# Optimization experiments

Measured on AMD Instinct MI355X. Metric: run time of the kernel, lower is better.

The kernel has to match this reference:

```python
import jax, jax.numpy as jnp
import numpy as np

DIM = 1024
H = 16
D = DIM // H  # head_dim = 64
SCALE = 1.0 / (D ** 0.5 * 1.0)  # 1/(sqrt(head_dim)*temperature)
MIN_CUTOFF = 1e-15


def setup_inputs() -> dict:
    key = jax.random.key(0)
    ks = jax.random.split(key, 6)
    B, T = 2, 2048
    x = jax.random.normal(ks[0], (B, T, DIM), dtype=jnp.float32)
    cutoffs = jax.random.uniform(ks[1], (B, T, T), dtype=jnp.float32)
    # torch nn.Linear params: weight [out, in], bias [out]
    W_qkv = jax.random.normal(ks[2], (3 * DIM, DIM), dtype=jnp.float32) * (DIM ** -0.5)
    b_qkv = jax.random.normal(ks[3], (3 * DIM,), dtype=jnp.float32) * 0.01
    W_out = jax.random.normal(ks[4], (DIM, DIM), dtype=jnp.float32) * (DIM ** -0.5)
    b_out = jax.random.normal(ks[5], (DIM,), dtype=jnp.float32) * 0.01
    return {"x": x, "cutoffs": cutoffs, "W_qkv": W_qkv, "b_qkv": b_qkv,
            "W_out": W_out, "b_out": b_out}


def reference(x, cutoffs, W_qkv, b_qkv, W_out, b_out):
    B, T, _ = x.shape
    # QKV projection -> [B, T, 3, H, D] -> [3, B, H, T, D]
    qkv = (jnp.einsum('btc,oc->bto', x, W_qkv) + b_qkv)
    qkv = qkv.reshape(B, T, 3, H, D).transpose(2, 0, 3, 1, 4)
    q, k, v = qkv[0], qkv[1], qkv[2]
    # additive log-bias from cutoffs, broadcast over heads
    bias = jnp.log(jnp.clip(cutoffs, MIN_CUTOFF, None))[:, None, :, :]  # [B,1,T,T]
    scores = jnp.einsum('bhqd,bhkd->bhqk', q, k) * SCALE + bias
    attn = jax.nn.softmax(scores, axis=-1)
    out = jnp.einsum('bhqk,bhkd->bhqd', attn, v)  # [B,H,T,D]
    out = out.transpose(0, 2, 1, 3).reshape(B, T, DIM)
    return jnp.einsum('btc,oc->bto', out, W_out) + b_out
```

## Files before the change

### kernel.cpp

```cpp
#include <hip/hip_runtime.h>

typedef __attribute__((ext_vector_type(4))) float f32x4;
typedef __attribute__((ext_vector_type(8))) short bf16x8;

__device__ __forceinline__ unsigned short f2bf(float f) {
    union { float f; unsigned u; } v; v.f = f;
    unsigned r = v.u + 0x7FFFu + ((v.u >> 16) & 1u);
    return (unsigned short)(r >> 16);
}
__device__ __forceinline__ float bf2f(unsigned short s) {
    union { unsigned u; float f; } v; v.u = ((unsigned)s) << 16;
    return v.f;
}

#define GLD16(gp, lp)                                                          \
    __builtin_amdgcn_global_load_lds(                                          \
        (const __attribute__((address_space(1))) void*)(gp),                   \
        (__attribute__((address_space(3))) void*)(lp), 16, 0, 0)

__global__ void k_cvt(const float* __restrict__ in, unsigned short* __restrict__ out, int n4) {
    int i = blockIdx.x * blockDim.x + threadIdx.x;
    int stride = gridDim.x * blockDim.x;
    for (; i < n4; i += stride) {
        float4 v = reinterpret_cast<const float4*>(in)[i];
        ushort4 o;
        o.x = f2bf(v.x); o.y = f2bf(v.y); o.z = f2bf(v.z); o.w = f2bf(v.w);
        reinterpret_cast<ushort4*>(out)[i] = o;
    }
}

__global__ void k_cvtc(const float* __restrict__ in, unsigned short* __restrict__ out, int n4) {
    int i = blockIdx.x * blockDim.x + threadIdx.x;
    int stride = gridDim.x * blockDim.x;
    for (; i < n4; i += stride) {
        float4 v = reinterpret_cast<const float4*>(in)[i];
        ushort4 o;
        o.x = f2bf(fmaxf(v.x, 1e-15f)); o.y = f2bf(fmaxf(v.y, 1e-15f));
        o.z = f2bf(fmaxf(v.z, 1e-15f)); o.w = f2bf(fmaxf(v.w, 1e-15f));
        reinterpret_cast<ushort4*>(out)[i] = o;
    }
}

template <int MODE>
__global__ __launch_bounds__(256) void gemm_bt(
    const unsigned short* __restrict__ A, const unsigned short* __restrict__ B,
    const float* __restrict__ bias, float* __restrict__ outf,
    unsigned short* __restrict__ qb, unsigned short* __restrict__ kb,
    unsigned short* __restrict__ vb, int M, int N, int K)
{
    __shared__ unsigned short sA[2][128 * 32];
    __shared__ unsigned short sB[2][128 * 32];
    const int tid = threadIdx.x;
    const int w = tid >> 6, lane = tid & 63, g = lane >> 4, r = lane & 15;
    const int tm = blockIdx.x * 128, tn = blockIdx.y * 128;
    const int wr = w >> 1, wc = w & 1;

    f32x4 acc[4][4];
#pragma unroll
    for (int i = 0; i < 4; i++)
#pragma unroll
        for (int j = 0; j < 4; j++) acc[i][j] = (f32x4)0.f;

    const unsigned short* ga0 = A + (size_t)(tm + w * 32 + (lane >> 2)) * K + (lane & 3) * 8;
    const unsigned short* gb0 = B + (size_t)(tn + w * 32 + (lane >> 2)) * K + (lane & 3) * 8;
    const int lbase = w * 32 * 32;

    auto stageAB = [&](int nb, int kk) {
        GLD16(ga0 + kk, &sA[nb][lbase]);
        GLD16(ga0 + kk + (size_t)16 * K, &sA[nb][lbase + 16 * 32]);
        GLD16(gb0 + kk, &sB[nb][lbase]);
        GLD16(gb0 + kk + (size_t)16 * K, &sB[nb][lbase + 16 * 32]);
    };

    stageAB(0, 0);
    __syncthreads();

#pragma unroll 2
    for (int kk = 0; kk < K; kk += 32) {
        const int cur = (kk >> 5) & 1;
        if (kk + 32 < K) stageAB(cur ^ 1, kk + 32);
        bf16x8 af[4], bfv[4];
#pragma unroll
        for (int f = 0; f < 4; f++) af[f] = *(const bf16x8*)&sA[cur][(wr * 64 + f * 16 + r) * 32 + g * 8];
#pragma unroll
        for (int f = 0; f < 4; f++) bfv[f] = *(const bf16x8*)&sB[cur][(wc * 64 + f * 16 + r) * 32 + g * 8];
#pragma unroll
        for (int i = 0; i < 4; i++)
#pragma unroll
            for (int j = 0; j < 4; j++)
                acc[i][j] = __builtin_amdgcn_mfma_f32_16x16x32_bf16(af[i], bfv[j], acc[i][j], 0, 0, 0);
        __syncthreads();
    }

#pragma unroll
    for (int fj = 0; fj < 4; fj++) {
        int n = tn + wc * 64 + fj * 16 + r;
        float bn = bias[n];
#pragma unroll
        for (int fi = 0; fi < 4; fi++) {
#pragma unroll
            for (int j = 0; j < 4; j++) {
                int m = tm + wr * 64 + fi * 16 + 4 * g + j;
                float v = acc[fi][fj][j] + bn;
                if (MODE == 0) {
                    outf[(size_t)m * N + n] = v;
                } else {
                    int three = n >> 10, h = (n >> 6) & 15, d = n & 63;
                    int b = m >> 11, t = m & 2047, bh = b * 16 + h;
                    if (three == 0) {
                        qb[((size_t)bh * 2048 + t) * 64 + d] = f2bf(v * 0.18033688f);
                    } else if (three == 1) {
                        kb[((size_t)bh * 2048 + t) * 64 + d] = f2bf(v);
                    } else {
                        vb[((size_t)bh * 64 + d) * 2048 + t] = f2bf(v);
                    }
                }
            }
        }
    }
}

__global__ __launch_bounds__(256) void attn_kernel(
    const unsigned short* __restrict__ qbuf, const unsigned short* __restrict__ kbuf,
    const unsigned short* __restrict__ vbuf, const unsigned short* __restrict__ cutb,
    unsigned short* __restrict__ outa)
{
    __shared__ unsigned short sK[64 * 64], sV[64 * 64], sP[4 * 16 * 64];
    const int tid = threadIdx.x, w = tid >> 6, lane = tid & 63, g = lane >> 4, r = lane & 15;
    const int qt = blockIdx.x, h = blockIdx.y, b = blockIdx.z;
    const int q0 = qt * 64, bh = b * 16 + h;

    bf16x8 aq[2];
    {
        const unsigned short* qp = qbuf + ((size_t)bh * 2048 + q0 + w * 16 + r) * 64;
        aq[0] = *(const bf16x8*)(qp + g * 8);
        aq[1] = *(const bf16x8*)(qp + 32 + g * 8);
    }

    const int c = lane & 7, rr = lane >> 3;
    auto stage = [&](int kt) {
#pragma unroll
        for (int i = 0; i < 2; i++) {
            int row = w * 16 + i * 8 + rr;
            GLD16(kbuf + ((size_t)bh * 2048 + kt * 64 + row) * 64 + (c ^ (row & 7)) * 8,
                  sK + (w * 16 + i * 8) * 64);
            GLD16(vbuf + ((size_t)bh * 64 + row) * 2048 + kt * 64 + (c ^ (row & 7)) * 8,
                  sV + (w * 16 + i * 8) * 64);
        }
    };

    const unsigned short* cp[4];
#pragma unroll
    for (int j = 0; j < 4; j++)
        cp[j] = cutb + ((size_t)b * 2048 + (q0 + w * 16 + 4 * g + j)) * 2048 + r;

    f32x4 oacc[4];
#pragma unroll
    for (int f = 0; f < 4; f++) oacc[f] = (f32x4)0.f;
    float psum[4] = {0.f, 0.f, 0.f, 0.f};

    unsigned short* sPw = sP + w * 16 * 64;

    for (int kt = 0; kt < 32; kt++) {
        __syncthreads();
        stage(kt);
        unsigned short cu[4][4];
#pragma unroll
        for (int f = 0; f < 4; f++)
#pragma unroll
            for (int j = 0; j < 4; j++) cu[f][j] = cp[j][kt * 64 + f * 16];
        __syncthreads();

        f32x4 sa[4];
#pragma unroll
        for (int f = 0; f < 4; f++) sa[f] = (f32x4)0.f;
#pragma unroll
        for (int s = 0; s < 2; s++)
#pragma unroll
            for (int f = 0; f < 4; f++) {
                int krow = f * 16 + r;
                bf16x8 bk = *(const bf16x8*)&sK[krow * 64 + ((s * 32 + g * 8) ^ ((krow & 7) << 3))];
                sa[f] = __builtin_amdgcn_mfma_f32_16x16x32_bf16(aq[s], bk, sa[f], 0, 0, 0);
            }

#pragma unroll
        for (int f = 0; f < 4; f++)
#pragma unroll
            for (int j = 0; j < 4; j++) {
                float p = bf2f(cu[f][j]) * exp2f(sa[f][j]);
                psum[j] += p;
                int row = 4 * g + j, col = f * 16 + r;
                sPw[row * 64 + (col ^ ((row & 7) << 3))] = f2bf(p);
            }

#pragma unroll
        for (int s = 0; s < 2; s++) {
            bf16x8 pa = *(const bf16x8*)&sPw[r * 64 + ((s * 32 + g * 8) ^ ((r & 7) << 3))];
#pragma unroll
            for (int f = 0; f < 4; f++) {
                int drow = f * 16 + r;
                bf16x8 bvv = *(const bf16x8*)&sV[drow * 64 + ((s * 32 + g * 8) ^ ((drow & 7) << 3))];
                oacc[f] = __builtin_amdgcn_mfma_f32_16x16x32_bf16(pa, bvv, oacc[f], 0, 0, 0);
            }
        }
    }

#pragma unroll
    for (int j = 0; j < 4; j++) {
        psum[j] += __shfl_xor(psum[j], 1);
        psum[j] += __shfl_xor(psum[j], 2);
        psum[j] += __shfl_xor(psum[j], 4);
        psum[j] += __shfl_xor(psum[j], 8);
    }

#pragma unroll
    for (int j = 0; j < 4; j++) {
        float inv = 1.f / psum[j];
        int q = q0 + w * 16 + 4 * g + j;
#pragma unroll
        for (int f = 0; f < 4; f++) {
            int d = f * 16 + r;
            outa[((size_t)(b * 2048 + q)) * 1024 + h * 64 + d] = f2bf(oacc[f][j] * inv);
        }
    }
}

extern "C" void kernel_launch(void* const* d_in, const int* in_sizes, int n_in,
                              void* d_out, int out_size, void* d_ws, size_t ws_size,
                              hipStream_t stream) {
    const float* x       = (const float*)d_in[0];
    const float* cutoffs = (const float*)d_in[1];
    const float* Wqkv    = (const float*)d_in[2];
    const float* bqkv    = (const float*)d_in[3];
    const float* Wout    = (const float*)d_in[4];
    const float* bout    = (const float*)d_in[5];
    float* out = (float*)d_out;

    char* ws = (char*)d_ws;
    unsigned short* x_bf    = (unsigned short*)ws;  ws += (size_t)4096 * 1024 * 2;
    unsigned short* wqkv_bf = (unsigned short*)ws;  ws += (size_t)3072 * 1024 * 2;
    unsigned short* wout_bf = (unsigned short*)ws;  ws += (size_t)1024 * 1024 * 2;
    unsigned short* qb      = (unsigned short*)ws;  ws += (size_t)32 * 2048 * 64 * 2;
    unsigned short* kb      = (unsigned short*)ws;  ws += (size_t)32 * 2048 * 64 * 2;
    unsigned short* vb      = (unsigned short*)ws;  ws += (size_t)32 * 2048 * 64 * 2;
    unsigned short* attn_o  = (unsigned short*)ws;  ws += (size_t)4096 * 1024 * 2;
    unsigned short* cutb    = (unsigned short*)ws;  ws += (size_t)2 * 2048 * 2048 * 2;

    k_cvt<<<1024, 256, 0, stream>>>(x,    x_bf,    4096 * 1024 / 4);
    k_cvt<<<1024, 256, 0, stream>>>(Wqkv, wqkv_bf, 3072 * 1024 / 4);
    k_cvt<<<512,  256, 0, stream>>>(Wout, wout_bf, 1024 * 1024 / 4);
    k_cvtc<<<2048, 256, 0, stream>>>(cutoffs, cutb, 2 * 2048 * 2048 / 4);

    gemm_bt<1><<<dim3(32, 24), 256, 0, stream>>>(x_bf, wqkv_bf, bqkv, nullptr,
                                                 qb, kb, vb, 4096, 3072, 1024);
    attn_kernel<<<dim3(32, 16, 2), 256, 0, stream>>>(qb, kb, vb, cutb, attn_o);
    gemm_bt<0><<<dim3(32, 8), 256, 0, stream>>>(attn_o, wout_bf, bout, out,
                                                nullptr, nullptr, nullptr, 4096, 1024, 1024);
}
```

Before: 255.5 us.

## Double-buffer K/V tiles in attention, add MFMA priority, shrink out-proj GEMM tile

The attention kernel now double-buffers its K and V shared-memory tiles, prefetching the next tile while computing on the current one. This removes one barrier per iteration and overlaps global loads with MFMA work. The GEMM keeps a single barrier per k-step and raises wave priority with s_setprio around the MFMA blocks. The output projection uses a 64-row M tile, giving 512 blocks instead of 256 for better CU coverage. In exchange, attention uses more LDS, which may lower occupancy, and the barrier moves to the top of the GEMM loop.

```diff
diff --git a/kernel.cpp b/kernel.cpp
--- a/kernel.cpp
+++ b/kernel.cpp
@@ -41,55 +41,59 @@
     }
 }
 
-template <int MODE>
+template <int MODE, int BM>
 __global__ __launch_bounds__(256) void gemm_bt(
     const unsigned short* __restrict__ A, const unsigned short* __restrict__ B,
     const float* __restrict__ bias, float* __restrict__ outf,
     unsigned short* __restrict__ qb, unsigned short* __restrict__ kb,
     unsigned short* __restrict__ vb, int M, int N, int K)
 {
-    __shared__ unsigned short sA[2][128 * 32];
+    constexpr int FM = BM / 32;
+    __shared__ unsigned short sA[2][BM * 32];
     __shared__ unsigned short sB[2][128 * 32];
     const int tid = threadIdx.x;
     const int w = tid >> 6, lane = tid & 63, g = lane >> 4, r = lane & 15;
-    const int tm = blockIdx.x * 128, tn = blockIdx.y * 128;
+    const int tm = blockIdx.x * BM, tn = blockIdx.y * 128;
     const int wr = w >> 1, wc = w & 1;
 
-    f32x4 acc[4][4];
-#pragma unroll
-    for (int i = 0; i < 4; i++)
+    f32x4 acc[FM][4];
+#pragma unroll
+    for (int i = 0; i < FM; i++)
 #pragma unroll
         for (int j = 0; j < 4; j++) acc[i][j] = (f32x4)0.f;
 
-    const unsigned short* ga0 = A + (size_t)(tm + w * 32 + (lane >> 2)) * K + (lane & 3) * 8;
+    const unsigned short* ga0 = A + (size_t)(tm + w * (BM / 4) + (lane >> 2)) * K + (lane & 3) * 8;
     const unsigned short* gb0 = B + (size_t)(tn + w * 32 + (lane >> 2)) * K + (lane & 3) * 8;
-    const int lbase = w * 32 * 32;
+    const int labase = w * (BM / 4) * 32;
+    const int lbbase = w * 32 * 32;
 
     auto stageAB = [&](int nb, int kk) {
-        GLD16(ga0 + kk, &sA[nb][lbase]);
-        GLD16(ga0 + kk + (size_t)16 * K, &sA[nb][lbase + 16 * 32]);
-        GLD16(gb0 + kk, &sB[nb][lbase]);
-        GLD16(gb0 + kk + (size_t)16 * K, &sB[nb][lbase + 16 * 32]);
+        GLD16(ga0 + kk, &sA[nb][labase]);
+        if (BM == 128) GLD16(ga0 + kk + (size_t)16 * K, &sA[nb][labase + 16 * 32]);
+        GLD16(gb0 + kk, &sB[nb][lbbase]);
+        GLD16(gb0 + kk + (size_t)16 * K, &sB[nb][lbbase + 16 * 32]);
     };
 
     stageAB(0, 0);
-    __syncthreads();
-
-#pragma unroll 2
+
     for (int kk = 0; kk < K; kk += 32) {
         const int cur = (kk >> 5) & 1;
+        __syncthreads();
         if (kk + 32 < K) stageAB(cur ^ 1, kk + 32);
-        bf16x8 af[4], bfv[4];
-#pragma unroll
-        for (int f = 0; f < 4; f++) af[f] = *(const bf16x8*)&sA[cur][(wr * 64 + f * 16 + r) * 32 + g * 8];
-#pragma unroll
-        for (int f = 0; f < 4; f++) bfv[f] = *(const bf16x8*)&sB[cur][(wc * 64 + f * 16 + r) * 32 + g * 8];
-#pragma unroll
-        for (int i = 0; i < 4; i++)
+        bf16x8 af[FM], bfv[4];
+#pragma unroll
+        for (int f = 0; f < FM; f++)
+            af[f] = *(const bf16x8*)&sA[cur][(wr * (BM / 2) + f * 16 + r) * 32 + g * 8];
+#pragma unroll
+        for (int f = 0; f < 4; f++)
+            bfv[f] = *(const bf16x8*)&sB[cur][(wc * 64 + f * 16 + r) * 32 + g * 8];
+        __builtin_amdgcn_s_setprio(1);
+#pragma unroll
+        for (int i = 0; i < FM; i++)
 #pragma unroll
             for (int j = 0; j < 4; j++)
                 acc[i][j] = __builtin_amdgcn_mfma_f32_16x16x32_bf16(af[i], bfv[j], acc[i][j], 0, 0, 0);
-        __syncthreads();
+        __builtin_amdgcn_s_setprio(0);
     }
 
 #pragma unroll
@@ -97,10 +101,10 @@
         int n = tn + wc * 64 + fj * 16 + r;
         float bn = bias[n];
 #pragma unroll
-        for (int fi = 0; fi < 4; fi++) {
+        for (int fi = 0; fi < FM; fi++) {
 #pragma unroll
             for (int j = 0; j < 4; j++) {
-                int m = tm + wr * 64 + fi * 16 + 4 * g + j;
+                int m = tm + wr * (BM / 2) + fi * 16 + 4 * g + j;
                 float v = acc[fi][fj][j] + bn;
                 if (MODE == 0) {
                     outf[(size_t)m * N + n] = v;
@@ -125,7 +129,7 @@
     const unsigned short* __restrict__ vbuf, const unsigned short* __restrict__ cutb,
     unsigned short* __restrict__ outa)
 {
-    __shared__ unsigned short sK[64 * 64], sV[64 * 64], sP[4 * 16 * 64];
+    __shared__ unsigned short sK[2][64 * 64], sV[2][64 * 64], sP[4][16 * 64];
     const int tid = threadIdx.x, w = tid >> 6, lane = tid & 63, g = lane >> 4, r = lane & 15;
     const int qt = blockIdx.x, h = blockIdx.y, b = blockIdx.z;
     const int q0 = qt * 64, bh = b * 16 + h;
@@ -138,14 +142,14 @@
     }
 
     const int c = lane & 7, rr = lane >> 3;
-    auto stage = [&](int kt) {
+    auto stage = [&](int nb, int kt) {
 #pragma unroll
         for (int i = 0; i < 2; i++) {
             int row = w * 16 + i * 8 + rr;
             GLD16(kbuf + ((size_t)bh * 2048 + kt * 64 + row) * 64 + (c ^ (row & 7)) * 8,
-                  sK + (w * 16 + i * 8) * 64);
+                  &sK[nb][(w * 16 + i * 8) * 64]);
             GLD16(vbuf + ((size_t)bh * 64 + row) * 2048 + kt * 64 + (c ^ (row & 7)) * 8,
-                  sV + (w * 16 + i * 8) * 64);
+                  &sV[nb][(w * 16 + i * 8) * 64]);
         }
     };
 
@@ -159,29 +163,34 @@
     for (int f = 0; f < 4; f++) oacc[f] = (f32x4)0.f;
     float psum[4] = {0.f, 0.f, 0.f, 0.f};
 
-    unsigned short* sPw = sP + w * 16 * 64;
+    unsigned short* sPw = sP[w];
+
+    stage(0, 0);
 
     for (int kt = 0; kt < 32; kt++) {
+        const int cur = kt & 1;
         __syncthreads();
-        stage(kt);
+        if (kt < 31) stage(cur ^ 1, kt + 1);
+
         unsigned short cu[4][4];
 #pragma unroll
         for (int f = 0; f < 4; f++)
 #pragma unroll
             for (int j = 0; j < 4; j++) cu[f][j] = cp[j][kt * 64 + f * 16];
-        __syncthreads();
 
         f32x4 sa[4];
 #pragma unroll
         for (int f = 0; f < 4; f++) sa[f] = (f32x4)0.f;
+        __builtin_amdgcn_s_setprio(1);
 #pragma unroll
         for (int s = 0; s < 2; s++)
 #pragma unroll
             for (int f = 0; f < 4; f++) {
                 int krow = f * 16 + r;
-                bf16x8 bk = *(const bf16x8*)&sK[krow * 64 + ((s * 32 + g * 8) ^ ((krow & 7) << 3))];
+                bf16x8 bk = *(const bf16x8*)&sK[cur][krow * 64 + ((s * 32 + g * 8) ^ ((krow & 7) << 3))];
                 sa[f] = __builtin_amdgcn_mfma_f32_16x16x32_bf16(aq[s], bk, sa[f], 0, 0, 0);
             }
+        __builtin_amdgcn_s_setprio(0);
 
 #pragma unroll
         for (int f = 0; f < 4; f++)
@@ -193,16 +202,18 @@
                 sPw[row * 64 + (col ^ ((row & 7) << 3))] = f2bf(p);
             }
 
+        __builtin_amdgcn_s_setprio(1);
 #pragma unroll
         for (int s = 0; s < 2; s++) {
             bf16x8 pa = *(const bf16x8*)&sPw[r * 64 + ((s * 32 + g * 8) ^ ((r & 7) << 3))];
 #pragma unroll
             for (int f = 0; f < 4; f++) {
                 int drow = f * 16 + r;
-                bf16x8 bvv = *(const bf16x8*)&sV[drow * 64 + ((s * 32 + g * 8) ^ ((drow & 7) << 3))];
+                bf16x8 bvv = *(const bf16x8*)&sV[cur][drow * 64 + ((s * 32 + g * 8) ^ ((drow & 7) << 3))];
                 oacc[f] = __builtin_amdgcn_mfma_f32_16x16x32_bf16(pa, bvv, oacc[f], 0, 0, 0);
             }
         }
+        __builtin_amdgcn_s_setprio(0);
     }
 
 #pragma unroll
@@ -251,9 +262,9 @@
     k_cvt<<<512,  256, 0, stream>>>(Wout, wout_bf, 1024 * 1024 / 4);
     k_cvtc<<<2048, 256, 0, stream>>>(cutoffs, cutb, 2 * 2048 * 2048 / 4);
 
-    gemm_bt<1><<<dim3(32, 24), 256, 0, stream>>>(x_bf, wqkv_bf, bqkv, nullptr,
-                                                 qb, kb, vb, 4096, 3072, 1024);
+    gemm_bt<1, 128><<<dim3(32, 24), 256, 0, stream>>>(x_bf, wqkv_bf, bqkv, nullptr,
+                                                      qb, kb, vb, 4096, 3072, 1024);
     attn_kernel<<<dim3(32, 16, 2), 256, 0, stream>>>(qb, kb, vb, cutb, attn_o);
-    gemm_bt<0><<<dim3(32, 8), 256, 0, stream>>>(attn_o, wout_bf, bout, out,
-                                                nullptr, nullptr, nullptr, 4096, 1024, 1024);
-}
+    gemm_bt<0, 64><<<dim3(64, 8), 256, 0, stream>>>(attn_o, wout_bf, bout, out,
+                                                    nullptr, nullptr, nullptr, 4096, 1024, 1024);
+}
```

Result: slower. 270.6 us (+5.9%).
